# Performance work log

Hardware: AMD Instinct MI355X
Metric: run time of the kernel (lower is better)

The kernel has to match this reference:

```python
import jax, jax.numpy as jnp
import numpy as np

IN_F = 4096
OUT_F = 4096
RANK = 8
NUM_EXPERTS = 64
TOP_K = 16
ROUTER_DIM = 16
ALPHA = 32
SCALING = ALPHA / TOP_K
BOTTLENECK = NUM_EXPERTS * RANK


def setup_inputs() -> dict:
    key = jax.random.key(0)
    ks = jax.random.split(key, 5)
    x = jax.random.normal(ks[0], (4, 4096, IN_F), dtype=jnp.float32)
    # kaiming-uniform-ish A, random B (zeros init would make output trivially 0)
    bound_a = float(np.sqrt(6.0 / IN_F))
    A_w = jax.random.uniform(ks[1], (BOTTLENECK, IN_F), jnp.float32, -bound_a, bound_a)
    B_w = jax.random.normal(ks[2], (OUT_F, BOTTLENECK), dtype=jnp.float32) * 0.02
    Wq_w = jax.random.normal(ks[3], (ROUTER_DIM, IN_F), dtype=jnp.float32) * 0.02
    keys = jax.random.normal(ks[4], (NUM_EXPERTS, ROUTER_DIM), dtype=jnp.float32) * 0.01
    return {"x": x, "A_w": A_w, "B_w": B_w, "Wq_w": Wq_w, "keys": keys}


def reference(x, A_w, B_w, Wq_w, keys):
    # lowrank router: q = x @ Wq^T, scores = q @ keys^T  -> [B,S,E]
    q = jnp.einsum('bsd,rd->bsr', x, Wq_w)
    scores = jnp.einsum('bsr,er->bse', q, keys)
    top_vals, top_idx = jax.lax.top_k(scores, TOP_K)          # [B,S,K]
    top_w = jax.nn.softmax(top_vals, axis=-1)                 # [B,S,K]
    # scatter weights into dense gate over experts [B,S,E]
    gate = jnp.sum(jax.nn.one_hot(top_idx, NUM_EXPERTS, dtype=top_w.dtype)
                   * top_w[..., None], axis=-2)
    # shared low-rank down-proj, gated per expert, up-proj
    z = jnp.einsum('bsd,nd->bsn', x, A_w)                     # [B,S,E*r]
    z = z.reshape(*z.shape[:-1], NUM_EXPERTS, RANK)
    z_gated = (z * gate[..., None]).reshape(*z.shape[:-2], BOTTLENECK)
    out = jnp.einsum('bsn,on->bso', z_gated, B_w) * SCALING
    return out
```

## Files before the change

kernel.cpp:

```cpp
#include <hip/hip_runtime.h>
#include <hip/hip_bf16.h>
#include <stdint.h>

#define IN_F 4096
#define OUT_F 4096
#define NE 64
#define TOPK 16
#define RD 16
#define BOT 512
#define NTOK 16384

typedef __attribute__((ext_vector_type(8))) short short8;
typedef __attribute__((ext_vector_type(4))) float floatx4;
typedef __attribute__((ext_vector_type(2))) double double2v;

__device__ __forceinline__ unsigned short f2bf_ru(float f) {
  unsigned int u = __float_as_uint(f);
  return (unsigned short)((u + 0x8000u) >> 16);
}
__device__ __forceinline__ unsigned short f2bf_rne(float f) {
  unsigned int u = __float_as_uint(f);
  return (unsigned short)((u + 0x7FFFu + ((u >> 16) & 1u)) >> 16);
}

__global__ __launch_bounds__(256) void prep_kernel(
    const float* __restrict__ A_w, const float* __restrict__ B_w,
    unsigned short* __restrict__ Abf, unsigned short* __restrict__ Bbf) {
  int i = blockIdx.x * 256 + threadIdx.x;
  if (i < BOT * IN_F) {
    Abf[i] = f2bf_rne(A_w[i]);
    Bbf[i] = f2bf_rne(B_w[i]);
  }
}

__global__ __launch_bounds__(256) void router_kernel(
    const float* __restrict__ x, const float* __restrict__ Wq,
    const float* __restrict__ keys, float* __restrict__ gate) {
  __shared__ double x_lds[32][132];
  __shared__ double wq_lds[16][132];
  __shared__ double q_lds[32][16];
  __shared__ double sc[32][64];
  const int tid = threadIdx.x;
  const size_t t0 = (size_t)blockIdx.x * 32;
  const int r = tid & 15, tg = tid >> 4;
  double acc0 = 0.0, acc1 = 0.0;

  for (int kc = 0; kc < IN_F; kc += 128) {
    __syncthreads();
    for (int i = 0; i < 4; i++) {
      int f = i * 256 + tid;
      int row = f >> 5, c = (f & 31) * 4;
      float4 v = *(const float4*)(x + (t0 + row) * IN_F + kc + c);
      x_lds[row][c] = (double)v.x; x_lds[row][c + 1] = (double)v.y;
      x_lds[row][c + 2] = (double)v.z; x_lds[row][c + 3] = (double)v.w;
    }
    for (int i = 0; i < 2; i++) {
      int f = i * 256 + tid;
      int row = f >> 5, c = (f & 31) * 4;
      float4 v = *(const float4*)(Wq + (size_t)row * IN_F + kc + c);
      wq_lds[row][c] = (double)v.x; wq_lds[row][c + 1] = (double)v.y;
      wq_lds[row][c + 2] = (double)v.z; wq_lds[row][c + 3] = (double)v.w;
    }
    __syncthreads();
    const double* xr0 = x_lds[tg * 2];
    const double* xr1 = x_lds[tg * 2 + 1];
    const double* wr = wq_lds[r];
#pragma unroll 8
    for (int k = 0; k < 128; k += 2) {
      double2v w = *(const double2v*)(wr + k);
      double2v a = *(const double2v*)(xr0 + k);
      double2v b = *(const double2v*)(xr1 + k);
      acc0 += a.x * w.x; acc0 += a.y * w.y;
      acc1 += b.x * w.x; acc1 += b.y * w.y;
    }
  }
  q_lds[tg * 2][r] = acc0;
  q_lds[tg * 2 + 1][r] = acc1;
  __syncthreads();

  {
    int t = tid >> 3, e0 = (tid & 7) * 8;
    for (int e = e0; e < e0 + 8; e++) {
      double s = 0.0;
      for (int rr = 0; rr < 16; rr++) s += q_lds[t][rr] * (double)keys[e * RD + rr];
      sc[t][e] = s;
    }
  }
  __syncthreads();

  if (tid < 32) {
    int t = tid;
    double vals[16]; int idx[16];
    unsigned long long used = 0ull;
    for (int s = 0; s < 16; s++) {
      double best = -1e300; int bi = 0;
      for (int e = 0; e < 64; e++) {
        double v = sc[t][e];
        if (!((used >> e) & 1ull) && v > best) { best = v; bi = e; }
      }
      used |= (1ull << bi);
      vals[s] = best; idx[s] = bi;
    }
    double mx = vals[0], sum = 0.0, w[16];
    for (int i = 0; i < 16; i++) { w[i] = exp(vals[i] - mx); sum += w[i]; }
    double inv = 1.0 / sum;
    float* grow = gate + (t0 + t) * NE;
    for (int e = 0; e < 64; e++) grow[e] = 0.0f;
    for (int i = 0; i < 16; i++) grow[idx[i]] = (float)(w[i] * inv);
  }
}

__global__ __launch_bounds__(256) void stageA_kernel(
    const float* __restrict__ x, const unsigned short* __restrict__ Abf,
    const float* __restrict__ gate, unsigned short* __restrict__ z) {
  __shared__ unsigned short As[128 * 32];
  __shared__ unsigned short Bs[128 * 32];
  __shared__ float gl[128 * 16];
  const int tid = threadIdx.x;
  const int bid = blockIdx.x;
  const int mt = (bid & 7) + (bid >> 5) * 8;
  const int nt = (bid >> 3) & 3;
  const size_t m0 = (size_t)mt * 128;
  const int n0 = nt * 128;

  for (int i = 0; i < 8; i++) {
    int f = i * 256 + tid;
    gl[f] = gate[(m0 + (f >> 4)) * NE + (n0 >> 3) + (f & 15)];
  }
  const int wid = tid >> 6, lane = tid & 63;
  const int wm = (wid & 1) * 64, wn = (wid >> 1) * 64;
  const int lr = lane & 15, lq = lane >> 4;
  floatx4 acc[4][4];
  for (int i = 0; i < 4; i++)
    for (int j = 0; j < 4; j++) acc[i][j] = 0.0f;

  for (int k0 = 0; k0 < IN_F; k0 += 32) {
    __syncthreads();
    {
      int c4 = (tid & 7) * 4;
      int rbase = tid >> 3;
      for (int p = 0; p < 4; p++) {
        int row = p * 32 + rbase;
        float4 v = *(const float4*)(x + (m0 + row) * IN_F + k0 + c4);
        ushort4 h;
        h.x = f2bf_ru(v.x); h.y = f2bf_ru(v.y);
        h.z = f2bf_ru(v.z); h.w = f2bf_ru(v.w);
        *(ushort4*)(As + row * 32 + c4) = h;
      }
    }
    for (int p = 0; p < 2; p++) {
      int f = p * 256 + tid;
      int row = f >> 2, c8 = (f & 3) * 8;
      float4 v = *(const float4*)(Abf + (size_t)(n0 + row) * IN_F + k0 + c8);
      *(float4*)(Bs + row * 32 + c8) = v;
    }
    __syncthreads();
    short8 a[4], b[4];
    for (int i = 0; i < 4; i++) a[i] = *(const short8*)(As + (wm + i * 16 + lr) * 32 + lq * 8);
    for (int j = 0; j < 4; j++) b[j] = *(const short8*)(Bs + (wn + j * 16 + lr) * 32 + lq * 8);
    for (int i = 0; i < 4; i++)
      for (int j = 0; j < 4; j++)
        acc[i][j] = __builtin_amdgcn_mfma_f32_16x16x32_bf16(a[i], b[j], acc[i][j], 0, 0, 0);
  }
  for (int i = 0; i < 4; i++) {
    for (int j = 0; j < 4; j++) {
      int cl = wn + j * 16 + lr;
      int el = cl >> 3;
      for (int g = 0; g < 4; g++) {
        int rl = wm + i * 16 + lq * 4 + g;
        float v = acc[i][j][g] * gl[rl * 16 + el];
        z[(m0 + rl) * BOT + n0 + cl] = f2bf_ru(v);
      }
    }
  }
}

__global__ __launch_bounds__(256) void stageB_kernel(
    const unsigned short* __restrict__ z, const unsigned short* __restrict__ Bbf,
    float* __restrict__ out) {
  __shared__ unsigned short As[128 * 32];
  __shared__ unsigned short Bs[128 * 32];
  const int tid = threadIdx.x;
  const int bid = blockIdx.x;
  const int mt = (bid & 7) + (bid >> 8) * 8;
  const int nt = (bid >> 3) & 31;
  const size_t m0 = (size_t)mt * 128;
  const int n0 = nt * 128;
  const int wid = tid >> 6, lane = tid & 63;
  const int wm = (wid & 1) * 64, wn = (wid >> 1) * 64;
  const int lr = lane & 15, lq = lane >> 4;
  floatx4 acc[4][4];
  for (int i = 0; i < 4; i++)
    for (int j = 0; j < 4; j++) acc[i][j] = 0.0f;

  for (int k0 = 0; k0 < BOT; k0 += 32) {
    __syncthreads();
    for (int p = 0; p < 2; p++) {
      int f = p * 256 + tid;
      int row = f >> 2, c8 = (f & 3) * 8;
      *(float4*)(As + row * 32 + c8) =
          *(const float4*)(z + (m0 + row) * BOT + k0 + c8);
      *(float4*)(Bs + row * 32 + c8) =
          *(const float4*)(Bbf + (size_t)(n0 + row) * BOT + k0 + c8);
    }
    __syncthreads();
    short8 a[4], b[4];
    for (int i = 0; i < 4; i++) a[i] = *(const short8*)(As + (wm + i * 16 + lr) * 32 + lq * 8);
    for (int j = 0; j < 4; j++) b[j] = *(const short8*)(Bs + (wn + j * 16 + lr) * 32 + lq * 8);
    for (int i = 0; i < 4; i++)
      for (int j = 0; j < 4; j++)
        acc[i][j] = __builtin_amdgcn_mfma_f32_16x16x32_bf16(a[i], b[j], acc[i][j], 0, 0, 0);
  }
  for (int i = 0; i < 4; i++) {
    for (int j = 0; j < 4; j++) {
      int cl = wn + j * 16 + lr;
      for (int g = 0; g < 4; g++) {
        int rl = wm + i * 16 + lq * 4 + g;
        out[(m0 + rl) * OUT_F + n0 + cl] = acc[i][j][g] * 2.0f;
      }
    }
  }
}

extern "C" void kernel_launch(void* const* d_in, const int* in_sizes, int n_in,
                              void* d_out, int out_size, void* d_ws, size_t ws_size,
                              hipStream_t stream) {
  const float* x    = (const float*)d_in[0];
  const float* A_w  = (const float*)d_in[1];
  const float* B_w  = (const float*)d_in[2];
  const float* Wq   = (const float*)d_in[3];
  const float* keys = (const float*)d_in[4];
  float* out = (float*)d_out;

  char* ws = (char*)d_ws;
  float* gate          = (float*)ws;
  unsigned short* z    = (unsigned short*)(ws + (4 << 20));
  unsigned short* Abf  = (unsigned short*)(ws + (4 << 20) + 16777216);
  unsigned short* Bbf  = Abf + BOT * IN_F;

  hipLaunchKernelGGL(prep_kernel, dim3(8192), dim3(256), 0, stream, A_w, B_w, Abf, Bbf);
  hipLaunchKernelGGL(router_kernel, dim3(512), dim3(256), 0, stream, x, Wq, keys, gate);
  hipLaunchKernelGGL(stageA_kernel, dim3(512), dim3(256), 0, stream, x, Abf, gate, z);
  hipLaunchKernelGGL(stageB_kernel, dim3(4096), dim3(256), 0, stream, z, Bbf, out);
}
```

Before: 800.0 us.

## Fuse x bf16 conversion into router, pad LDS rows, vectorize weight prep

The router now converts x to bf16 while it streams x, writing the result into the output buffer as scratch. stageA then loads pre-converted bf16 x instead of converting fp32 on every tile. The router is also restructured: each thread keeps register accumulators for all 16 router dims over column slices, reduces them with cross-lane shuffles, and caches keys in LDS. LDS tiles in both GEMMs are padded to a row stride of 40 to cut bank conflicts, prep is vectorized with float4, and z rounding switches to round-to-nearest-even. Using the output buffer as scratch works only because stageB overwrites it afterwards.

```diff
diff --git a/kernel.cpp b/kernel.cpp
--- a/kernel.cpp
+++ b/kernel.cpp
@@ -5,19 +5,13 @@
 #define IN_F 4096
 #define OUT_F 4096
 #define NE 64
-#define TOPK 16
 #define RD 16
 #define BOT 512
 #define NTOK 16384
 
 typedef __attribute__((ext_vector_type(8))) short short8;
 typedef __attribute__((ext_vector_type(4))) float floatx4;
-typedef __attribute__((ext_vector_type(2))) double double2v;
-
-__device__ __forceinline__ unsigned short f2bf_ru(float f) {
-  unsigned int u = __float_as_uint(f);
-  return (unsigned short)((u + 0x8000u) >> 16);
-}
+
 __device__ __forceinline__ unsigned short f2bf_rne(float f) {
   unsigned int u = __float_as_uint(f);
   return (unsigned short)((u + 0x7FFFu + ((u >> 16) & 1u)) >> 16);
@@ -26,65 +20,106 @@
 __global__ __launch_bounds__(256) void prep_kernel(
     const float* __restrict__ A_w, const float* __restrict__ B_w,
     unsigned short* __restrict__ Abf, unsigned short* __restrict__ Bbf) {
-  int i = blockIdx.x * 256 + threadIdx.x;
-  if (i < BOT * IN_F) {
-    Abf[i] = f2bf_rne(A_w[i]);
-    Bbf[i] = f2bf_rne(B_w[i]);
+  int i4 = blockIdx.x * 256 + threadIdx.x;
+  if (i4 < (BOT * IN_F) / 4) {
+    float4 a = ((const float4*)A_w)[i4];
+    float4 b = ((const float4*)B_w)[i4];
+    ushort4 ha, hb;
+    ha.x = f2bf_rne(a.x); ha.y = f2bf_rne(a.y); ha.z = f2bf_rne(a.z); ha.w = f2bf_rne(a.w);
+    hb.x = f2bf_rne(b.x); hb.y = f2bf_rne(b.y); hb.z = f2bf_rne(b.z); hb.w = f2bf_rne(b.w);
+    ((ushort4*)Abf)[i4] = ha;
+    ((ushort4*)Bbf)[i4] = hb;
   }
 }
 
 __global__ __launch_bounds__(256) void router_kernel(
     const float* __restrict__ x, const float* __restrict__ Wq,
-    const float* __restrict__ keys, float* __restrict__ gate) {
-  __shared__ double x_lds[32][132];
-  __shared__ double wq_lds[16][132];
-  __shared__ double q_lds[32][16];
-  __shared__ double sc[32][64];
+    const float* __restrict__ keys, float* __restrict__ gate,
+    unsigned short* __restrict__ x_bf) {
+  __shared__ double wq_sc[16 * 256];
+  __shared__ double q_s[32 * 17];
+  __shared__ double keys_s[64 * 16];
   const int tid = threadIdx.x;
+  const int tg = tid >> 4, kl = tid & 15;
   const size_t t0 = (size_t)blockIdx.x * 32;
-  const int r = tid & 15, tg = tid >> 4;
-  double acc0 = 0.0, acc1 = 0.0;
-
-  for (int kc = 0; kc < IN_F; kc += 128) {
-    __syncthreads();
-    for (int i = 0; i < 4; i++) {
+  const int ta = tg * 2, tb = ta + 1;
+
+  for (int i = tid; i < NE * RD; i += 256) keys_s[i] = (double)keys[i];
+
+  double acc[2][16];
+#pragma unroll
+  for (int r = 0; r < 16; r++) { acc[0][r] = 0.0; acc[1][r] = 0.0; }
+
+  const float* xa = x + (t0 + ta) * IN_F;
+  const float* xb = x + (t0 + tb) * IN_F;
+  unsigned short* xba = x_bf + (t0 + ta) * IN_F;
+  unsigned short* xbb = x_bf + (t0 + tb) * IN_F;
+
+  for (int kc = 0; kc < IN_F; kc += 256) {
+    __syncthreads();
+#pragma unroll
+    for (int i = 0; i < 16; i++) {
       int f = i * 256 + tid;
-      int row = f >> 5, c = (f & 31) * 4;
-      float4 v = *(const float4*)(x + (t0 + row) * IN_F + kc + c);
-      x_lds[row][c] = (double)v.x; x_lds[row][c + 1] = (double)v.y;
-      x_lds[row][c + 2] = (double)v.z; x_lds[row][c + 3] = (double)v.w;
-    }
-    for (int i = 0; i < 2; i++) {
-      int f = i * 256 + tid;
-      int row = f >> 5, c = (f & 31) * 4;
-      float4 v = *(const float4*)(Wq + (size_t)row * IN_F + kc + c);
-      wq_lds[row][c] = (double)v.x; wq_lds[row][c + 1] = (double)v.y;
-      wq_lds[row][c + 2] = (double)v.z; wq_lds[row][c + 3] = (double)v.w;
-    }
-    __syncthreads();
-    const double* xr0 = x_lds[tg * 2];
-    const double* xr1 = x_lds[tg * 2 + 1];
-    const double* wr = wq_lds[r];
-#pragma unroll 8
-    for (int k = 0; k < 128; k += 2) {
-      double2v w = *(const double2v*)(wr + k);
-      double2v a = *(const double2v*)(xr0 + k);
-      double2v b = *(const double2v*)(xr1 + k);
-      acc0 += a.x * w.x; acc0 += a.y * w.y;
-      acc1 += b.x * w.x; acc1 += b.y * w.y;
-    }
-  }
-  q_lds[tg * 2][r] = acc0;
-  q_lds[tg * 2 + 1][r] = acc1;
+      int row = f >> 8, col = f & 255;
+      wq_sc[f] = (double)Wq[row * IN_F + kc + col];
+    }
+    __syncthreads();
+#pragma unroll
+    for (int s = 0; s < 8; s++) {
+      int c = kc + s * 32 + kl * 2;
+      float2 va = *(const float2*)(xa + c);
+      float2 vb = *(const float2*)(xb + c);
+      ushort2 ha, hb;
+      ha.x = f2bf_rne(va.x); ha.y = f2bf_rne(va.y);
+      hb.x = f2bf_rne(vb.x); hb.y = f2bf_rne(vb.y);
+      *(ushort2*)(xba + c) = ha;
+      *(ushort2*)(xbb + c) = hb;
+      double a0 = (double)va.x, a1 = (double)va.y;
+      double b0 = (double)vb.x, b1 = (double)vb.y;
+      const double* wp = wq_sc + s * 32 + kl * 2;
+#pragma unroll
+      for (int r = 0; r < 16; r++) {
+        double w0 = wp[r * 256], w1 = wp[r * 256 + 1];
+        acc[0][r] += a0 * w0 + a1 * w1;
+        acc[1][r] += b0 * w0 + b1 * w1;
+      }
+    }
+  }
+#pragma unroll
+  for (int m = 1; m <= 8; m <<= 1) {
+#pragma unroll
+    for (int r = 0; r < 16; r++) {
+      acc[0][r] += __shfl_xor(acc[0][r], m, 64);
+      acc[1][r] += __shfl_xor(acc[1][r], m, 64);
+    }
+  }
+  if (kl == 0) {
+#pragma unroll
+    for (int r = 0; r < 16; r++) {
+      q_s[ta * 17 + r] = acc[0][r];
+      q_s[tb * 17 + r] = acc[1][r];
+    }
+  }
   __syncthreads();
 
+  double* sc = wq_sc;
   {
-    int t = tid >> 3, e0 = (tid & 7) * 8;
-    for (int e = e0; e < e0 + 8; e++) {
+    int t = tid & 31, eg = tid >> 5;
+    double q[16];
+#pragma unroll
+    for (int r = 0; r < 16; r++) q[r] = q_s[t * 17 + r];
+    for (int i = 0; i < 8; i++) {
+      int e = eg * 8 + i;
       double s = 0.0;
-      for (int rr = 0; rr < 16; rr++) s += q_lds[t][rr] * (double)keys[e * RD + rr];
-      sc[t][e] = s;
-    }
+#pragma unroll
+      for (int r = 0; r < 16; r++) s += q[r] * keys_s[e * 16 + r];
+      sc[t * 65 + e] = s;
+    }
+  }
+  {
+    float4 z4 = make_float4(0.f, 0.f, 0.f, 0.f);
+    float4* grow4 = (float4*)(gate + t0 * NE);
+    for (int i = tid; i < 32 * NE / 4; i += 256) grow4[i] = z4;
   }
   __syncthreads();
 
@@ -95,7 +130,7 @@
     for (int s = 0; s < 16; s++) {
       double best = -1e300; int bi = 0;
       for (int e = 0; e < 64; e++) {
-        double v = sc[t][e];
+        double v = sc[t * 65 + e];
         if (!((used >> e) & 1ull) && v > best) { best = v; bi = e; }
       }
       used |= (1ull << bi);
@@ -104,17 +139,16 @@
     double mx = vals[0], sum = 0.0, w[16];
     for (int i = 0; i < 16; i++) { w[i] = exp(vals[i] - mx); sum += w[i]; }
     double inv = 1.0 / sum;
-    float* grow = gate + (t0 + t) * NE;
-    for (int e = 0; e < 64; e++) grow[e] = 0.0f;
-    for (int i = 0; i < 16; i++) grow[idx[i]] = (float)(w[i] * inv);
+    float* gr = gate + (t0 + t) * NE;
+    for (int i = 0; i < 16; i++) gr[idx[i]] = (float)(w[i] * inv);
   }
 }
 
 __global__ __launch_bounds__(256) void stageA_kernel(
-    const float* __restrict__ x, const unsigned short* __restrict__ Abf,
+    const unsigned short* __restrict__ x_bf, const unsigned short* __restrict__ Abf,
     const float* __restrict__ gate, unsigned short* __restrict__ z) {
-  __shared__ unsigned short As[128 * 32];
-  __shared__ unsigned short Bs[128 * 32];
+  __shared__ unsigned short As[128 * 40];
+  __shared__ unsigned short Bs[128 * 40];
   __shared__ float gl[128 * 16];
   const int tid = threadIdx.x;
   const int bid = blockIdx.x;
@@ -136,28 +170,18 @@
 
   for (int k0 = 0; k0 < IN_F; k0 += 32) {
     __syncthreads();
-    {
-      int c4 = (tid & 7) * 4;
-      int rbase = tid >> 3;
-      for (int p = 0; p < 4; p++) {
-        int row = p * 32 + rbase;
-        float4 v = *(const float4*)(x + (m0 + row) * IN_F + k0 + c4);
-        ushort4 h;
-        h.x = f2bf_ru(v.x); h.y = f2bf_ru(v.y);
-        h.z = f2bf_ru(v.z); h.w = f2bf_ru(v.w);
-        *(ushort4*)(As + row * 32 + c4) = h;
-      }
-    }
     for (int p = 0; p < 2; p++) {
       int f = p * 256 + tid;
       int row = f >> 2, c8 = (f & 3) * 8;
-      float4 v = *(const float4*)(Abf + (size_t)(n0 + row) * IN_F + k0 + c8);
-      *(float4*)(Bs + row * 32 + c8) = v;
+      *(float4*)(As + row * 40 + c8) =
+          *(const float4*)(x_bf + (m0 + row) * IN_F + k0 + c8);
+      *(float4*)(Bs + row * 40 + c8) =
+          *(const float4*)(Abf + (size_t)(n0 + row) * IN_F + k0 + c8);
     }
     __syncthreads();
     short8 a[4], b[4];
-    for (int i = 0; i < 4; i++) a[i] = *(const short8*)(As + (wm + i * 16 + lr) * 32 + lq * 8);
-    for (int j = 0; j < 4; j++) b[j] = *(const short8*)(Bs + (wn + j * 16 + lr) * 32 + lq * 8);
+    for (int i = 0; i < 4; i++) a[i] = *(const short8*)(As + (wm + i * 16 + lr) * 40 + lq * 8);
+    for (int j = 0; j < 4; j++) b[j] = *(const short8*)(Bs + (wn + j * 16 + lr) * 40 + lq * 8);
     for (int i = 0; i < 4; i++)
       for (int j = 0; j < 4; j++)
         acc[i][j] = __builtin_amdgcn_mfma_f32_16x16x32_bf16(a[i], b[j], acc[i][j], 0, 0, 0);
@@ -169,7 +193,7 @@
       for (int g = 0; g < 4; g++) {
         int rl = wm + i * 16 + lq * 4 + g;
         float v = acc[i][j][g] * gl[rl * 16 + el];
-        z[(m0 + rl) * BOT + n0 + cl] = f2bf_ru(v);
+        z[(m0 + rl) * BOT + n0 + cl] = f2bf_rne(v);
       }
     }
   }
@@ -178,8 +202,8 @@
 __global__ __launch_bounds__(256) void stageB_kernel(
     const unsigned short* __restrict__ z, const unsigned short* __restrict__ Bbf,
     float* __restrict__ out) {
-  __shared__ unsigned short As[128 * 32];
-  __shared__ unsigned short Bs[128 * 32];
+  __shared__ unsigned short As[128 * 40];
+  __shared__ unsigned short Bs[128 * 40];
   const int tid = threadIdx.x;
   const int bid = blockIdx.x;
   const int mt = (bid & 7) + (bid >> 8) * 8;
@@ -198,15 +222,15 @@
     for (int p = 0; p < 2; p++) {
       int f = p * 256 + tid;
       int row = f >> 2, c8 = (f & 3) * 8;
-      *(float4*)(As + row * 32 + c8) =
+      *(float4*)(As + row * 40 + c8) =
           *(const float4*)(z + (m0 + row) * BOT + k0 + c8);
-      *(float4*)(Bs + row * 32 + c8) =
+      *(float4*)(Bs + row * 40 + c8) =
           *(const float4*)(Bbf + (size_t)(n0 + row) * BOT + k0 + c8);
     }
     __syncthreads();
     short8 a[4], b[4];
-    for (int i = 0; i < 4; i++) a[i] = *(const short8*)(As + (wm + i * 16 + lr) * 32 + lq * 8);
-    for (int j = 0; j < 4; j++) b[j] = *(const short8*)(Bs + (wn + j * 16 + lr) * 32 + lq * 8);
+    for (int i = 0; i < 4; i++) a[i] = *(const short8*)(As + (wm + i * 16 + lr) * 40 + lq * 8);
+    for (int j = 0; j < 4; j++) b[j] = *(const short8*)(Bs + (wn + j * 16 + lr) * 40 + lq * 8);
     for (int i = 0; i < 4; i++)
       for (int j = 0; j < 4; j++)
         acc[i][j] = __builtin_amdgcn_mfma_f32_16x16x32_bf16(a[i], b[j], acc[i][j], 0, 0, 0);
@@ -237,9 +261,10 @@
   unsigned short* z    = (unsigned short*)(ws + (4 << 20));
   unsigned short* Abf  = (unsigned short*)(ws + (4 << 20) + 16777216);
   unsigned short* Bbf  = Abf + BOT * IN_F;
-
-  hipLaunchKernelGGL(prep_kernel, dim3(8192), dim3(256), 0, stream, A_w, B_w, Abf, Bbf);
-  hipLaunchKernelGGL(router_kernel, dim3(512), dim3(256), 0, stream, x, Wq, keys, gate);
-  hipLaunchKernelGGL(stageA_kernel, dim3(512), dim3(256), 0, stream, x, Abf, gate, z);
+  unsigned short* x_bf = (unsigned short*)d_out;
+
+  hipLaunchKernelGGL(prep_kernel, dim3(2048), dim3(256), 0, stream, A_w, B_w, Abf, Bbf);
+  hipLaunchKernelGGL(router_kernel, dim3(512), dim3(256), 0, stream, x, Wq, keys, gate, x_bf);
+  hipLaunchKernelGGL(stageA_kernel, dim3(512), dim3(256), 0, stream, x_bf, Abf, gate, z);
   hipLaunchKernelGGL(stageB_kernel, dim3(4096), dim3(256), 0, stream, z, Bbf, out);
 }
```

Result: slower. 844.0 us (+5.5%).
